# Optimization experiments

Hardware: AMD Instinct MI355X
Metric: run time of the kernel (lower is better)

## Reference

```python
import jax, jax.numpy as jnp
import numpy as np

N_NODES = 50000
N_EDGES = 800000
N_GRAPHS = 512
IN_DIM, HID_DIM, EMB_DIM = 128, 256, 128
EPS = 1e-5


def setup_inputs() -> dict:
    key = jax.random.key(0)
    ks = jax.random.split(key, 12)
    x = jax.random.normal(ks[0], (N_NODES, IN_DIM), dtype=jnp.float32)
    edge_index = jax.random.randint(ks[1], (2, N_EDGES), 0, N_NODES, dtype=jnp.int32)
    batch = jnp.sort(jax.random.randint(ks[2], (N_NODES,), 0, N_GRAPHS, dtype=jnp.int32))
    s1 = 1.0 / np.sqrt(IN_DIM)
    s2 = 1.0 / np.sqrt(HID_DIM)
    return {
        "x": x,
        "edge_index": edge_index,
        "batch": batch,
        "W1": jax.random.uniform(ks[3], (IN_DIM, HID_DIM), jnp.float32, -s1, s1),
        "b1": jnp.zeros((HID_DIM,), jnp.float32),
        "gamma1": jnp.ones((HID_DIM,), jnp.float32),
        "beta1": jnp.zeros((HID_DIM,), jnp.float32),
        "W2": jax.random.uniform(ks[4], (HID_DIM, EMB_DIM), jnp.float32, -s2, s2),
        "b2": jnp.zeros((EMB_DIM,), jnp.float32),
        "gamma2": jnp.ones((EMB_DIM,), jnp.float32),
        "beta2": jnp.zeros((EMB_DIM,), jnp.float32),
    }


def _gcn_conv(x, W, b, src, dst, n_nodes):
    # PyG GCNConv: h = xW; aggregate with sym-normalized adjacency incl. self-loops; + bias
    h = x @ W  # [N, D]
    ones = jnp.ones(src.shape[0], dtype=h.dtype)
    deg = jax.ops.segment_sum(ones, dst, num_segments=n_nodes) + 1.0  # self-loop
    dinv = jax.lax.rsqrt(deg)
    norm = dinv[src] * dinv[dst]  # [E]
    msg = h[src] * norm[:, None]  # gather + scale  [E, D]
    agg = jax.ops.segment_sum(msg, dst, num_segments=n_nodes)
    agg = agg + h * (1.0 / deg)[:, None]  # self-loop contribution (norm = 1/deg)
    return agg + b


def _batchnorm(h, gamma, beta):
    mean = jnp.mean(h, axis=0)
    var = jnp.mean(jnp.square(h - mean), axis=0)  # biased, training mode
    return gamma * (h - mean) * jax.lax.rsqrt(var + EPS) + beta


def reference(x, edge_index, batch, W1, b1, gamma1, beta1, W2, b2, gamma2, beta2):
    src, dst = edge_index[0], edge_index[1]
    n = x.shape[0]
    h = _gcn_conv(x, W1, b1, src, dst, n)
    h = _batchnorm(jax.nn.relu(h), gamma1, beta1)
    h = _gcn_conv(h, W2, b2, src, dst, n)
    h = _batchnorm(jax.nn.relu(h), gamma2, beta2)
    return jax.ops.segment_max(h, batch, num_segments=N_GRAPHS)
```

## Files before the change

### kernel.cpp

```cpp
#include <hip/hip_runtime.h>
#include <math.h>

#define N_NODES 50000
#define N_EDGES 800000
#define N_GRAPHS 512
#define IN_DIM 128
#define HID_DIM 256
#define EMB_DIM 128
#define EPS 1e-5f
#define ELLW 64
#define NV4 (N_EDGES / 4)
#define NB 196
#define CAP 8192
#define PA_BLOCKS 512
#define CPB ((NV4 + PA_BLOCKS - 1) / PA_BLOCKS)
#define F2B_N (N_NODES * IN_DIM / 4)
#define F2B_BLOCKS ((F2B_N + 255) / 256)
#define TW1_BLOCKS ((HID_DIM * IN_DIM + 255) / 256)
#define NSLOTS 128
#define GSLOTS 128
#define AG_BLOCKS ((N_NODES + 63) / 64)

typedef __attribute__((ext_vector_type(8))) short bf16x8;
typedef __attribute__((ext_vector_type(4))) float f32x4;
typedef __attribute__((ext_vector_type(4))) int i32x4;
typedef __attribute__((ext_vector_type(4))) unsigned short u16x4;

static __device__ __forceinline__ unsigned short f2b(float f) {
    unsigned u = __float_as_uint(f);
    return (unsigned short)((u + 0x7fffu + ((u >> 16) & 1u)) >> 16);
}
static __device__ __forceinline__ float dinv_of(int d) {
    return rsqrtf((float)(min(d, ELLW) + 1));
}

__global__ void __launch_bounds__(256) scatter_convert(const int* __restrict__ src,
                                                       const int* __restrict__ dst,
                                                       int* __restrict__ gcur,
                                                       int* __restrict__ bucketbuf,
                                                       const float* __restrict__ x,
                                                       unsigned short* __restrict__ xbf,
                                                       const float* __restrict__ W1,
                                                       unsigned short* __restrict__ W1t) {
    int b = blockIdx.x;
    if (b < PA_BLOCKS) {
        __shared__ int hcnt[NB], hbase[NB], loff[NB];
        int t = threadIdx.x;
        for (int j = t; j < NB; j += 256) { hcnt[j] = 0; loff[j] = 0; }
        __syncthreads();
        int base = b * CPB;
        int i_end = min(base + CPB, NV4);
        const i32x4* dst4 = (const i32x4*)dst;
        const i32x4* src4 = (const i32x4*)src;
        int i0 = base + t, i1 = base + 256 + t;
        bool val0 = i0 < i_end, val1 = i1 < i_end;
        i32x4 d0 = {0, 0, 0, 0}, s0 = {0, 0, 0, 0};
        i32x4 d1 = {0, 0, 0, 0}, s1 = {0, 0, 0, 0};
        if (val0) {
            d0 = __builtin_nontemporal_load(&dst4[i0]);
            s0 = __builtin_nontemporal_load(&src4[i0]);
        }
        if (val1) {
            d1 = __builtin_nontemporal_load(&dst4[i1]);
            s1 = __builtin_nontemporal_load(&src4[i1]);
        }
        if (val0) {
#pragma unroll
            for (int e = 0; e < 4; ++e) atomicAdd(&hcnt[d0[e] >> 8], 1);
        }
        if (val1) {
#pragma unroll
            for (int e = 0; e < 4; ++e) atomicAdd(&hcnt[d1[e] >> 8], 1);
        }
        __syncthreads();
        for (int j = t; j < NB; j += 256) {
            int c = hcnt[j];
            if (c) hbase[j] = atomicAdd(&gcur[j], c);
        }
        __syncthreads();
        if (val0) {
#pragma unroll
            for (int e = 0; e < 4; ++e) {
                int d = d0[e], bk = d >> 8;
                int o = atomicAdd(&loff[bk], 1);
                int idx = hbase[bk] + o;
                if (idx < CAP) bucketbuf[bk * CAP + idx] = ((d & 255) << 16) | s0[e];
            }
        }
        if (val1) {
#pragma unroll
            for (int e = 0; e < 4; ++e) {
                int d = d1[e], bk = d >> 8;
                int o = atomicAdd(&loff[bk], 1);
                int idx = hbase[bk] + o;
                if (idx < CAP) bucketbuf[bk * CAP + idx] = ((d & 255) << 16) | s1[e];
            }
        }
    } else if (b < PA_BLOCKS + F2B_BLOCKS) {
        int i = (b - PA_BLOCKS) * 256 + threadIdx.x;
        if (i < F2B_N) {
            f32x4 v = __builtin_nontemporal_load(&((const f32x4*)x)[i]);
            u16x4 o;
            o[0] = f2b(v[0]); o[1] = f2b(v[1]); o[2] = f2b(v[2]); o[3] = f2b(v[3]);
            __builtin_nontemporal_store(o, &((u16x4*)xbf)[i]);
        }
    } else {
        int j = (b - PA_BLOCKS - F2B_BLOCKS) * 256 + threadIdx.x;
        if (j < HID_DIM * IN_DIM) {
            int n = j >> 7;
            int k = j & 127;
            W1t[j] = f2b(W1[k * HID_DIM + n]);
        }
    }
}

__global__ void __launch_bounds__(256) build_ell(const int* __restrict__ gcur,
                                                 const int* __restrict__ bucketbuf,
                                                 int* __restrict__ fill,
                                                 int* __restrict__ col) {
    __shared__ unsigned short lcol[256 * ELLW];
    __shared__ int lfill[256];
    int b = blockIdx.x;
    int t = threadIdx.x;
    lfill[t] = 0;
    __syncthreads();
    int n = min(gcur[b], CAP);
    const int* buf = bucketbuf + b * CAP;
    for (int i = t; i < n; i += 256) {
        int p = buf[i];
        int dl = p >> 16;
        int pos = atomicAdd(&lfill[dl], 1);
        if (pos < ELLW) lcol[(dl << 6) + pos] = (unsigned short)(p & 0xFFFF);
    }
    __syncthreads();
    int v = (b << 8) + t;
    if (v < N_NODES) fill[v] = lfill[t];
    for (int idx4 = t; idx4 < 256 * (ELLW / 4); idx4 += 256) {
        int row = idx4 >> 4;
        int vv = (b << 8) + row;
        if (vv < N_NODES) {
            int c0 = (idx4 & 15) << 2;
            u16x4 w = *(const u16x4*)&lcol[(row << 6) + c0];
            int4 o4 = make_int4(w[0], w[1], w[2], w[3]);
            *(int4*)&col[((size_t)vv << 6) + c0] = o4;
        }
    }
}

static __device__ __forceinline__ void acc8(float* acc, uint4 r, float w) {
    const unsigned* u = (const unsigned*)&r;
#pragma unroll
    for (int k = 0; k < 4; ++k) {
        float lo = __uint_as_float((u[k] & 0xFFFFu) << 16);
        float hi = __uint_as_float(u[k] & 0xFFFF0000u);
        acc[2 * k]     += w * lo;
        acc[2 * k + 1] += w * hi;
    }
}

__global__ void __launch_bounds__(256) fused_aggemm1(const unsigned short* __restrict__ xbf,
                                                     const int* __restrict__ deg,
                                                     const int* __restrict__ col,
                                                     const unsigned short* __restrict__ W1t,
                                                     const float* __restrict__ bias,
                                                     unsigned short* __restrict__ y1,
                                                     float* __restrict__ sums,
                                                     float* __restrict__ sumsqs) {
    const int LDA = 136;
    __shared__ unsigned short As[64 * LDA];
    __shared__ float sred[4][2][16];
    __shared__ float qred[4][2][16];
    int tid = threadIdx.x;
    int lane = tid & 63;
    int w = tid >> 6;
    int grpw = lane >> 4;
    int p = lane & 15;
    int grp = tid >> 4;
    int bm = blockIdx.x * 64;
    int sl = grpw << 4;

#pragma unroll
    for (int it = 0; it < 4; ++it) {
        int vl = grp + (it << 4);
        int v = bm + vl;
        float o[8] = {};
        if (v < N_NODES) {
            int dcl = min(deg[v], ELLW);
            uint4 selfr = *(const uint4*)(xbf + (size_t)v * 128 + p * 8);
            float acc[8] = {};
            for (int sel = 0; sel < 4; ++sel) {
                int base = sel * 16;
                if (base >= dcl) break;
                int idx = base + p;
                int cidx = min(idx, dcl - 1);
                int u_l = col[((size_t)v << 6) + cidx];
                float w_l = (idx < dcl) ? dinv_of(deg[u_l]) : 0.f;
                int n = min(16, dcl - base);
                for (int e0 = 0; e0 < n; e0 += 4) {
                    int u0 = __shfl(u_l, sl + e0, 64);
                    int u1 = __shfl(u_l, sl + e0 + 1, 64);
                    int u2 = __shfl(u_l, sl + e0 + 2, 64);
                    int u3 = __shfl(u_l, sl + e0 + 3, 64);
                    float w0 = __shfl(w_l, sl + e0, 64);
                    float w1 = __shfl(w_l, sl + e0 + 1, 64);
                    float w2 = __shfl(w_l, sl + e0 + 2, 64);
                    float w3 = __shfl(w_l, sl + e0 + 3, 64);
                    uint4 d0 = *(const uint4*)(xbf + (size_t)u0 * 128 + p * 8);
                    uint4 d1 = *(const uint4*)(xbf + (size_t)u1 * 128 + p * 8);
                    uint4 d2 = *(const uint4*)(xbf + (size_t)u2 * 128 + p * 8);
                    uint4 d3 = *(const uint4*)(xbf + (size_t)u3 * 128 + p * 8);
                    acc8(acc, d0, w0);
                    acc8(acc, d1, w1);
                    acc8(acc, d2, w2);
                    acc8(acc, d3, w3);
                }
            }
            const unsigned* su = (const unsigned*)&selfr;
            float dv = rsqrtf((float)(dcl + 1));
            float dv2 = dv * dv;
#pragma unroll
            for (int k = 0; k < 4; ++k) {
                float lo = __uint_as_float((su[k] & 0xFFFFu) << 16);
                float hi = __uint_as_float(su[k] & 0xFFFF0000u);
                o[2 * k]     = dv * acc[2 * k]     + lo * dv2;
                o[2 * k + 1] = dv * acc[2 * k + 1] + hi * dv2;
            }
        }
        uint4 packed;
        unsigned* pu = (unsigned*)&packed;
#pragma unroll
        for (int k = 0; k < 4; ++k)
            pu[k] = (unsigned)f2b(o[2 * k]) | ((unsigned)f2b(o[2 * k + 1]) << 16);
        *(uint4*)&As[vl * LDA + p * 8] = packed;
    }
    __syncthreads();

    int wr = (w >> 1) * 32, wc = (w & 1) * 32;
    int l15 = lane & 15, q = lane >> 4;
    for (int s = 0; s < 4; ++s) {
        f32x4 acc2[2][2] = {};
        const unsigned short* Bbase = W1t + (size_t)(s * 64 + wc) * 128;
#pragma unroll
        for (int k0 = 0; k0 < 128; k0 += 32) {
            bf16x8 a0 = *(const bf16x8*)&As[(wr + 0 + l15) * LDA + k0 + q * 8];
            bf16x8 a1 = *(const bf16x8*)&As[(wr + 16 + l15) * LDA + k0 + q * 8];
            bf16x8 b0 = *(const bf16x8*)(Bbase + (size_t)(0 + l15) * 128 + k0 + q * 8);
            bf16x8 b1 = *(const bf16x8*)(Bbase + (size_t)(16 + l15) * 128 + k0 + q * 8);
            acc2[0][0] = __builtin_amdgcn_mfma_f32_16x16x32_bf16(a0, b0, acc2[0][0], 0, 0, 0);
            acc2[0][1] = __builtin_amdgcn_mfma_f32_16x16x32_bf16(a0, b1, acc2[0][1], 0, 0, 0);
            acc2[1][0] = __builtin_amdgcn_mfma_f32_16x16x32_bf16(a1, b0, acc2[1][0], 0, 0, 0);
            acc2[1][1] = __builtin_amdgcn_mfma_f32_16x16x32_bf16(a1, b1, acc2[1][1], 0, 0, 0);
        }
        float scol[2] = {0.f, 0.f};
        float qcol[2] = {0.f, 0.f};
#pragma unroll
        for (int mi = 0; mi < 2; ++mi)
#pragma unroll
            for (int ni = 0; ni < 2; ++ni) {
                int colc = s * 64 + wc + ni * 16 + l15;
                float bv = bias[colc];
#pragma unroll
                for (int r = 0; r < 4; ++r) {
                    int row = bm + wr + mi * 16 + q * 4 + r;
                    if (row < N_NODES) {
                        float vv = acc2[mi][ni][r] + bv;
                        vv = fmaxf(vv, 0.f);
                        y1[(size_t)row * HID_DIM + colc] = f2b(vv);
                        scol[ni] += vv; qcol[ni] += vv * vv;
                    }
                }
            }
#pragma unroll
        for (int ni = 0; ni < 2; ++ni) {
            float ss = scol[ni], qq = qcol[ni];
            ss += __shfl_xor(ss, 16, 64);
            ss += __shfl_xor(ss, 32, 64);
            qq += __shfl_xor(qq, 16, 64);
            qq += __shfl_xor(qq, 32, 64);
            if (lane < 16) { sred[w][ni][l15] = ss; qred[w][ni][l15] = qq; }
        }
        __syncthreads();
        if (tid < 64) {
            int par = (tid >> 5) & 1;
            int ni = (tid >> 4) & 1;
            int l = tid & 15;
            int slot = blockIdx.x & (GSLOTS - 1);
            atomicAdd(&sums[slot * HID_DIM + s * 64 + tid],
                      sred[par][ni][l] + sred[par + 2][ni][l]);
            atomicAdd(&sumsqs[slot * HID_DIM + s * 64 + tid],
                      qred[par][ni][l] + qred[par + 2][ni][l]);
        }
        __syncthreads();
    }
}

template <bool RELU, bool OUT_BF, bool BIAS, bool STATS>
__global__ void __launch_bounds__(256) aggw_kernel(const unsigned short* __restrict__ h,
                                                   const int* __restrict__ deg,
                                                   const int* __restrict__ col,
                                                   const float* __restrict__ bias,
                                                   void* __restrict__ y,
                                                   float* __restrict__ sumP,
                                                   float* __restrict__ sqP) {
    __shared__ float sv[STATS ? 16 : 1][STATS ? 128 : 1];
    int tid = threadIdx.x;
    int lane = tid & 63;
    int grpw = lane >> 4;
    int p = lane & 15;
    int grp = tid >> 4;
    int v = blockIdx.x * 16 + grp;

    int dcl = min(deg[v], ELLW);
    uint4 selfr = *(const uint4*)(h + (size_t)v * 128 + p * 8);

    float acc[8] = {};
    int sl = grpw << 4;
#pragma unroll 4
    for (int sel = 0; sel < 4; ++sel) {
        int base = sel * 16;
        if (base >= dcl) break;
        int idx = base + p;
        int cidx = min(idx, dcl - 1);
        int u_l = col[(v << 6) + cidx];
        float w_l = (idx < dcl) ? dinv_of(deg[u_l]) : 0.f;
        int n = min(16, dcl - base);
        for (int e0 = 0; e0 < n; e0 += 4) {
            int u0 = __shfl(u_l, sl + e0, 64);
            int u1 = __shfl(u_l, sl + e0 + 1, 64);
            int u2 = __shfl(u_l, sl + e0 + 2, 64);
            int u3 = __shfl(u_l, sl + e0 + 3, 64);
            float w0 = __shfl(w_l, sl + e0, 64);
            float w1 = __shfl(w_l, sl + e0 + 1, 64);
            float w2 = __shfl(w_l, sl + e0 + 2, 64);
            float w3 = __shfl(w_l, sl + e0 + 3, 64);
            uint4 d0 = *(const uint4*)(h + (size_t)u0 * 128 + p * 8);
            uint4 d1 = *(const uint4*)(h + (size_t)u1 * 128 + p * 8);
            uint4 d2 = *(const uint4*)(h + (size_t)u2 * 128 + p * 8);
            uint4 d3 = *(const uint4*)(h + (size_t)u3 * 128 + p * 8);
            acc8(acc, d0, w0);
            acc8(acc, d1, w1);
            acc8(acc, d2, w2);
            acc8(acc, d3, w3);
        }
    }

    {
        const unsigned* su = (const unsigned*)&selfr;
        float dv = rsqrtf((float)(dcl + 1));
        float dv2 = dv * dv;
        float o[8];
#pragma unroll
        for (int k = 0; k < 4; ++k) {
            float lo = __uint_as_float((su[k] & 0xFFFFu) << 16);
            float hi = __uint_as_float(su[k] & 0xFFFF0000u);
            o[2 * k]     = dv * acc[2 * k]     + lo * dv2;
            o[2 * k + 1] = dv * acc[2 * k + 1] + hi * dv2;
        }
        if (BIAS) {
            float4 bv0 = *(const float4*)&bias[p * 8];
            float4 bv1 = *(const float4*)&bias[p * 8 + 4];
            o[0] += bv0.x; o[1] += bv0.y; o[2] += bv0.z; o[3] += bv0.w;
            o[4] += bv1.x; o[5] += bv1.y; o[6] += bv1.z; o[7] += bv1.w;
        }
        if (RELU) {
#pragma unroll
            for (int k = 0; k < 8; ++k) o[k] = fmaxf(o[k], 0.f);
        }
        if (OUT_BF) {
            uint4 packed;
            unsigned* pu = (unsigned*)&packed;
#pragma unroll
            for (int k = 0; k < 4; ++k)
                pu[k] = (unsigned)f2b(o[2 * k]) | ((unsigned)f2b(o[2 * k + 1]) << 16);
            *(uint4*)((unsigned short*)y + (size_t)v * 128 + p * 8) = packed;
        } else {
            float* yf = (float*)y + (size_t)v * 128 + p * 8;
            *(float4*)yf = make_float4(o[0], o[1], o[2], o[3]);
            *(float4*)(yf + 4) = make_float4(o[4], o[5], o[6], o[7]);
        }
        if (STATS) {
#pragma unroll
            for (int k = 0; k < 8; ++k) sv[grp][p * 8 + k] = o[k];
        }
    }

    if (STATS) {
        __syncthreads();
        if (tid < 128) {
            float s = 0.f, q = 0.f;
#pragma unroll
            for (int r = 0; r < 16; ++r) {
                float val = sv[r][tid];
                s += val;
                q += val * val;
            }
            int slot = blockIdx.x & (NSLOTS - 1);
            atomicAdd(&sumP[slot * 128 + tid], s);
            atomicAdd(&sqP[slot * 128 + tid], q);
        }
    }
}

template <bool RELU, bool STATS>
__global__ void __launch_bounds__(256) mfma_gemm_kernel(const unsigned short* __restrict__ A,
                                                        const unsigned short* __restrict__ Bt,
                                                        const float* __restrict__ bias,
                                                        unsigned short* __restrict__ C,
                                                        float* __restrict__ sums,
                                                        float* __restrict__ sumsqs,
                                                        int M, int N, int K) {
    const int LDT = 40;
    __shared__ unsigned short As[64 * LDT];
    __shared__ unsigned short Bs[64 * LDT];
    int tid = threadIdx.x;
    int bm = blockIdx.x * 64;
    int bn = blockIdx.y * 64;
    int lr = tid >> 2;
    int lc = (tid & 3) * 8;
    int lane = tid & 63;
    int w = tid >> 6;
    int wr = (w >> 1) * 32, wc = (w & 1) * 32;
    int l15 = lane & 15, q = lane >> 4;

    f32x4 acc[2][2] = {};
    bool arow_ok = (bm + lr) < M;
    const unsigned short* Aptr = A + (size_t)(bm + lr) * K + lc;
    const unsigned short* Bptr = Bt + (size_t)(bn + lr) * K + lc;

    uint4 av = arow_ok ? *(const uint4*)(Aptr) : make_uint4(0u, 0u, 0u, 0u);
    uint4 bv = *(const uint4*)(Bptr);

    for (int k0 = 0; k0 < K; k0 += 32) {
        *(uint4*)&As[lr * LDT + lc] = av;
        *(uint4*)&Bs[lr * LDT + lc] = bv;
        __syncthreads();
        if (k0 + 32 < K) {
            av = arow_ok ? *(const uint4*)(Aptr + k0 + 32) : make_uint4(0u, 0u, 0u, 0u);
            bv = *(const uint4*)(Bptr + k0 + 32);
        }
        bf16x8 a0 = *(const bf16x8*)&As[(wr + 0 + l15) * LDT + q * 8];
        bf16x8 a1 = *(const bf16x8*)&As[(wr + 16 + l15) * LDT + q * 8];
        bf16x8 b0 = *(const bf16x8*)&Bs[(wc + 0 + l15) * LDT + q * 8];
        bf16x8 b1 = *(const bf16x8*)&Bs[(wc + 16 + l15) * LDT + q * 8];
        acc[0][0] = __builtin_amdgcn_mfma_f32_16x16x32_bf16(a0, b0, acc[0][0], 0, 0, 0);
        acc[0][1] = __builtin_amdgcn_mfma_f32_16x16x32_bf16(a0, b1, acc[0][1], 0, 0, 0);
        acc[1][0] = __builtin_amdgcn_mfma_f32_16x16x32_bf16(a1, b0, acc[1][0], 0, 0, 0);
        acc[1][1] = __builtin_amdgcn_mfma_f32_16x16x32_bf16(a1, b1, acc[1][1], 0, 0, 0);
        __syncthreads();
    }

#pragma unroll
    for (int mi = 0; mi < 2; ++mi)
#pragma unroll
        for (int ni = 0; ni < 2; ++ni) {
            int colc = bn + wc + ni * 16 + l15;
            float bv2 = bias ? bias[colc] : 0.f;
#pragma unroll
            for (int r = 0; r < 4; ++r) {
                int row = bm + wr + mi * 16 + q * 4 + r;
                if (row < M) {
                    float vv = acc[mi][ni][r] + bv2;
                    if (RELU) vv = fmaxf(vv, 0.f);
                    C[(size_t)row * N + colc] = f2b(vv);
                }
            }
        }
}

__global__ void __launch_bounds__(256) prep2_kernel(const float* __restrict__ sum1P,
                                                    const float* __restrict__ sumsq1P,
                                                    const float* __restrict__ gamma1,
                                                    const float* __restrict__ beta1,
                                                    const float* __restrict__ W2,
                                                    unsigned short* __restrict__ W2pt,
                                                    float* __restrict__ bc2) {
    __shared__ float a1s[HID_DIM], s1s[HID_DIM];
    __shared__ float bp[16][17];
    int t = threadIdx.x;
    {
        float s = 0.f, q = 0.f;
#pragma unroll 8
        for (int j = 0; j < GSLOTS; ++j) {
            s += sum1P[j * HID_DIM + t];
            q += sumsq1P[j * HID_DIM + t];
        }
        float m = s * (1.f / N_NODES);
        float var = q * (1.f / N_NODES) - m * m;
        float a = gamma1[t] * rsqrtf(var + EPS);
        a1s[t] = a;
        s1s[t] = beta1[t] - m * a;
    }
    __syncthreads();
    int row = blockIdx.x * 16 + (t & 15);
    int ks = t >> 4;
    float bacc = 0.f;
    unsigned short wloc[16];
#pragma unroll
    for (int j = 0; j < 16; ++j) {
        int k = ks * 16 + j;
        float wv = W2[k * EMB_DIM + row];
        wloc[j] = f2b(a1s[k] * wv);
        bacc += s1s[k] * wv;
    }
    *(uint4*)&W2pt[(size_t)row * HID_DIM + ks * 16]     = *(uint4*)&wloc[0];
    *(uint4*)&W2pt[(size_t)row * HID_DIM + ks * 16 + 8] = *(uint4*)&wloc[8];
    bp[t & 15][ks] = bacc;
    __syncthreads();
    if (t < 16) {
        float s = 0.f;
#pragma unroll
        for (int g = 0; g < 16; ++g) s += bp[t][g];
        bc2[blockIdx.x * 16 + t] = s;
    }
}

__global__ void __launch_bounds__(128) segmax_kernel(const float* __restrict__ y,
                                                     const float* __restrict__ sumP,
                                                     const float* __restrict__ sqP,
                                                     const float* __restrict__ gamma2,
                                                     const float* __restrict__ beta2,
                                                     const int* __restrict__ batch,
                                                     float* __restrict__ out) {
    __shared__ int sh[2];
    int g = blockIdx.x;
    int c = threadIdx.x;
    float s2 = 0.f, q2 = 0.f;
#pragma unroll 8
    for (int j = 0; j < NSLOTS; ++j) {
        s2 += sumP[j * 128 + c];
        q2 += sqP[j * 128 + c];
    }
    float mch = s2 * (1.f / N_NODES);
    float var = q2 * (1.f / N_NODES) - mch * mch;
    float ac = gamma2[c] * rsqrtf(var + EPS);
    float sc = beta2[c] - mch * ac;
    if (threadIdx.x == 0) {
        int lo = 0, hi = N_NODES;
        while (lo < hi) { int mid = (lo + hi) >> 1; if (batch[mid] < g) lo = mid + 1; else hi = mid; }
        sh[0] = lo;
        hi = N_NODES;
        while (lo < hi) { int mid = (lo + hi) >> 1; if (batch[mid] < g + 1) lo = mid + 1; else hi = mid; }
        sh[1] = lo;
    }
    __syncthreads();
    int beg = sh[0], end = sh[1];
    float m = -INFINITY;
    for (int v = beg; v < end; ++v) {
        m = fmaxf(m, fmaf(ac, y[(size_t)v * EMB_DIM + c], sc));
    }
    out[(size_t)g * EMB_DIM + c] = m;
}

extern "C" void kernel_launch(void* const* d_in, const int* in_sizes, int n_in,
                              void* d_out, int out_size, void* d_ws, size_t ws_size,
                              hipStream_t stream) {
    const float* x      = (const float*)d_in[0];
    const int*   ei     = (const int*)d_in[1];
    const int*   batch  = (const int*)d_in[2];
    const float* W1     = (const float*)d_in[3];
    const float* b1     = (const float*)d_in[4];
    const float* gamma1 = (const float*)d_in[5];
    const float* beta1  = (const float*)d_in[6];
    const float* W2     = (const float*)d_in[7];
    const float* b2     = (const float*)d_in[8];
    const float* gamma2 = (const float*)d_in[9];
    const float* beta2  = (const float*)d_in[10];
    float* out = (float*)d_out;

    char* ws = (char*)d_ws;
    size_t off = 0;
    auto alloc = [&](size_t bytes) -> char* {
        char* p = ws + off;
        off = (off + bytes + 255) & ~(size_t)255;
        return p;
    };
    int*   gcur    = (int*)alloc((size_t)NB * 4);
    float* gsumP   = (float*)alloc((size_t)GSLOTS * HID_DIM * 4);
    float* gsqP    = (float*)alloc((size_t)GSLOTS * HID_DIM * 4);
    float* sumP    = (float*)alloc((size_t)NSLOTS * 128 * 4);
    float* sqP     = (float*)alloc((size_t)NSLOTS * 128 * 4);
    size_t zbytes = off;
    int*   fill   = (int*)alloc((size_t)N_NODES * 4);
    int*   bucketbuf = (int*)alloc((size_t)NB * CAP * 4);
    int*   col    = (int*)alloc((size_t)N_NODES * ELLW * 4);
    float* bc2    = (float*)alloc((size_t)EMB_DIM * 4);
    unsigned short* W1t  = (unsigned short*)alloc((size_t)HID_DIM * IN_DIM * 2);
    unsigned short* W2pt = (unsigned short*)alloc((size_t)HID_DIM * EMB_DIM * 2);
    unsigned short* xbf  = (unsigned short*)alloc((size_t)N_NODES * IN_DIM * 2);
    unsigned short* y1bf = (unsigned short*)alloc((size_t)N_NODES * HID_DIM * 2);
    unsigned short* gbf  = (unsigned short*)alloc((size_t)N_NODES * EMB_DIM * 2);
    float* y2 = (float*)xbf;
    (void)ws_size; (void)in_sizes; (void)n_in; (void)out_size;

    const int* src  = ei;
    const int* dstp = ei + N_EDGES;

    hipMemsetAsync(ws, 0, zbytes, stream);

    scatter_convert<<<PA_BLOCKS + F2B_BLOCKS + TW1_BLOCKS, 256, 0, stream>>>(
        src, dstp, gcur, bucketbuf, x, xbf, W1, W1t);
    build_ell<<<NB, 256, 0, stream>>>(gcur, bucketbuf, fill, col);

    fused_aggemm1<<<AG_BLOCKS, 256, 0, stream>>>(xbf, fill, col, W1t, b1, y1bf,
                                                 gsumP, gsqP);

    prep2_kernel<<<8, 256, 0, stream>>>(gsumP, gsqP, gamma1, beta1, W2, W2pt, bc2);

    dim3 g2((N_NODES + 63) / 64, EMB_DIM / 64);
    mfma_gemm_kernel<false, false><<<g2, 256, 0, stream>>>(y1bf, W2pt, bc2, gbf,
                                                           nullptr, nullptr,
                                                           N_NODES, EMB_DIM, HID_DIM);
    aggw_kernel<true, false, true, true><<<N_NODES / 16, 256, 0, stream>>>(
        gbf, fill, col, b2, y2, sumP, sqP);

    segmax_kernel<<<N_GRAPHS, 128, 0, stream>>>(y2, sumP, sqP,
                                                gamma2, beta2, batch, out);
}
```

Before: 264.5 us.

## Use 512 threads in fused aggregate-GEMM1 and drop per-slice block syncs

Doubles the block size of the fused first-layer aggregate+GEMM kernel so each thread aggregates two nodes instead of four. In the GEMM, each of the 8 waves now covers a 32x64 output tile over the full 256 columns in one pass, instead of looping over four 64-column slices. BatchNorm statistics are reduced with wave shuffles and atomically added per wave, which removes the shared-memory reduction and its two __syncthreads per slice. This gives more parallelism per block and fewer barriers, at the cost of more accumulator registers per thread and twice as many atomics to the statistics slots.

```diff
diff --git a/kernel.cpp b/kernel.cpp
--- a/kernel.cpp
+++ b/kernel.cpp
@@ -158,7 +158,7 @@
     }
 }
 
-__global__ void __launch_bounds__(256) fused_aggemm1(const unsigned short* __restrict__ xbf,
+__global__ void __launch_bounds__(512) fused_aggemm1(const unsigned short* __restrict__ xbf,
                                                      const int* __restrict__ deg,
                                                      const int* __restrict__ col,
                                                      const unsigned short* __restrict__ W1t,
@@ -168,20 +168,17 @@
                                                      float* __restrict__ sumsqs) {
     const int LDA = 136;
     __shared__ unsigned short As[64 * LDA];
-    __shared__ float sred[4][2][16];
-    __shared__ float qred[4][2][16];
     int tid = threadIdx.x;
     int lane = tid & 63;
     int w = tid >> 6;
-    int grpw = lane >> 4;
     int p = lane & 15;
     int grp = tid >> 4;
     int bm = blockIdx.x * 64;
-    int sl = grpw << 4;
-
-#pragma unroll
-    for (int it = 0; it < 4; ++it) {
-        int vl = grp + (it << 4);
+    int sl = (lane >> 4) << 4;
+
+#pragma unroll
+    for (int it = 0; it < 2; ++it) {
+        int vl = grp + (it << 5);
         int v = bm + vl;
         float o[8] = {};
         if (v < N_NODES) {
@@ -235,62 +232,48 @@
     }
     __syncthreads();
 
-    int wr = (w >> 1) * 32, wc = (w & 1) * 32;
+    int wr = (w & 1) * 32;
+    int wcg = (w >> 1) * 64;
     int l15 = lane & 15, q = lane >> 4;
-    for (int s = 0; s < 4; ++s) {
-        f32x4 acc2[2][2] = {};
-        const unsigned short* Bbase = W1t + (size_t)(s * 64 + wc) * 128;
-#pragma unroll
-        for (int k0 = 0; k0 < 128; k0 += 32) {
-            bf16x8 a0 = *(const bf16x8*)&As[(wr + 0 + l15) * LDA + k0 + q * 8];
-            bf16x8 a1 = *(const bf16x8*)&As[(wr + 16 + l15) * LDA + k0 + q * 8];
-            bf16x8 b0 = *(const bf16x8*)(Bbase + (size_t)(0 + l15) * 128 + k0 + q * 8);
-            bf16x8 b1 = *(const bf16x8*)(Bbase + (size_t)(16 + l15) * 128 + k0 + q * 8);
-            acc2[0][0] = __builtin_amdgcn_mfma_f32_16x16x32_bf16(a0, b0, acc2[0][0], 0, 0, 0);
-            acc2[0][1] = __builtin_amdgcn_mfma_f32_16x16x32_bf16(a0, b1, acc2[0][1], 0, 0, 0);
-            acc2[1][0] = __builtin_amdgcn_mfma_f32_16x16x32_bf16(a1, b0, acc2[1][0], 0, 0, 0);
-            acc2[1][1] = __builtin_amdgcn_mfma_f32_16x16x32_bf16(a1, b1, acc2[1][1], 0, 0, 0);
-        }
-        float scol[2] = {0.f, 0.f};
-        float qcol[2] = {0.f, 0.f};
-#pragma unroll
-        for (int mi = 0; mi < 2; ++mi)
-#pragma unroll
-            for (int ni = 0; ni < 2; ++ni) {
-                int colc = s * 64 + wc + ni * 16 + l15;
-                float bv = bias[colc];
-#pragma unroll
-                for (int r = 0; r < 4; ++r) {
-                    int row = bm + wr + mi * 16 + q * 4 + r;
-                    if (row < N_NODES) {
-                        float vv = acc2[mi][ni][r] + bv;
-                        vv = fmaxf(vv, 0.f);
-                        y1[(size_t)row * HID_DIM + colc] = f2b(vv);
-                        scol[ni] += vv; qcol[ni] += vv * vv;
-                    }
+    f32x4 acc2[2][4] = {};
+#pragma unroll
+    for (int k0 = 0; k0 < 128; k0 += 32) {
+        bf16x8 a0 = *(const bf16x8*)&As[(wr + 0 + l15) * LDA + k0 + q * 8];
+        bf16x8 a1 = *(const bf16x8*)&As[(wr + 16 + l15) * LDA + k0 + q * 8];
+#pragma unroll
+        for (int ni = 0; ni < 4; ++ni) {
+            bf16x8 b = *(const bf16x8*)(W1t + (size_t)(wcg + ni * 16 + l15) * 128 + k0 + q * 8);
+            acc2[0][ni] = __builtin_amdgcn_mfma_f32_16x16x32_bf16(a0, b, acc2[0][ni], 0, 0, 0);
+            acc2[1][ni] = __builtin_amdgcn_mfma_f32_16x16x32_bf16(a1, b, acc2[1][ni], 0, 0, 0);
+        }
+    }
+    int slot = blockIdx.x & (GSLOTS - 1);
+#pragma unroll
+    for (int ni = 0; ni < 4; ++ni) {
+        int colc = wcg + ni * 16 + l15;
+        float bv = bias[colc];
+        float scol = 0.f, qcol = 0.f;
+#pragma unroll
+        for (int mi = 0; mi < 2; ++mi) {
+#pragma unroll
+            for (int r = 0; r < 4; ++r) {
+                int row = bm + wr + mi * 16 + q * 4 + r;
+                if (row < N_NODES) {
+                    float vv = acc2[mi][ni][r] + bv;
+                    vv = fmaxf(vv, 0.f);
+                    y1[(size_t)row * HID_DIM + colc] = f2b(vv);
+                    scol += vv; qcol += vv * vv;
                 }
             }
-#pragma unroll
-        for (int ni = 0; ni < 2; ++ni) {
-            float ss = scol[ni], qq = qcol[ni];
-            ss += __shfl_xor(ss, 16, 64);
-            ss += __shfl_xor(ss, 32, 64);
-            qq += __shfl_xor(qq, 16, 64);
-            qq += __shfl_xor(qq, 32, 64);
-            if (lane < 16) { sred[w][ni][l15] = ss; qred[w][ni][l15] = qq; }
-        }
-        __syncthreads();
-        if (tid < 64) {
-            int par = (tid >> 5) & 1;
-            int ni = (tid >> 4) & 1;
-            int l = tid & 15;
-            int slot = blockIdx.x & (GSLOTS - 1);
-            atomicAdd(&sums[slot * HID_DIM + s * 64 + tid],
-                      sred[par][ni][l] + sred[par + 2][ni][l]);
-            atomicAdd(&sumsqs[slot * HID_DIM + s * 64 + tid],
-                      qred[par][ni][l] + qred[par + 2][ni][l]);
-        }
-        __syncthreads();
+        }
+        scol += __shfl_xor(scol, 16, 64);
+        scol += __shfl_xor(scol, 32, 64);
+        qcol += __shfl_xor(qcol, 16, 64);
+        qcol += __shfl_xor(qcol, 32, 64);
+        if (lane < 16) {
+            atomicAdd(&sums[slot * HID_DIM + colc], scol);
+            atomicAdd(&sumsqs[slot * HID_DIM + colc], qcol);
+        }
     }
 }
 
@@ -601,7 +584,7 @@
         src, dstp, gcur, bucketbuf, x, xbf, W1, W1t);
     build_ell<<<NB, 256, 0, stream>>>(gcur, bucketbuf, fill, col);
 
-    fused_aggemm1<<<AG_BLOCKS, 256, 0, stream>>>(xbf, fill, col, W1t, b1, y1bf,
+    fused_aggemm1<<<AG_BLOCKS, 512, 0, stream>>>(xbf, fill, col, W1t, b1, y1bf,
                                                  gsumP, gsqP);
 
     prep2_kernel<<<8, 256, 0, stream>>>(gsumP, gsqP, gamma1, beta1, W2, W2pt, bc2);
```

Measured after the change: 269.6 us. No clear change (+1.9%).
